# Performance work log

Measured on AMD Instinct MI355X. Metric: run time of the kernel, lower is better.

## Reference

```python
import jax, jax.numpy as jnp
import numpy as np

# CondInst DynamicMaskHead dims (defaults from cfg)
N_IMG, C_IN, H, W = 2, 8, 100, 152
N_INST = 500
CHANNELS = 8
STRIDE = 8  # mask_feat_stride (P3)
WEIGHT_NUMS = [(C_IN + 2) * CHANNELS, CHANNELS * CHANNELS, CHANNELS]  # [80, 64, 8]
BIAS_NUMS = [CHANNELS, CHANNELS, 1]
NUM_PARAMS = sum(WEIGHT_NUMS) + sum(BIAS_NUMS)  # 169


def setup_inputs() -> dict:
    key = jax.random.key(0)
    k1, k2, k3, k4, k5 = jax.random.split(key, 5)
    mask_feats = jax.random.normal(k1, (N_IMG, C_IN, H, W), jnp.float32)
    mask_head_params = jax.random.normal(k2, (N_INST, NUM_PARAMS), jnp.float32) * 0.1
    # instance centers in input-image pixel coords
    instance_locations = jax.random.uniform(k3, (N_INST, 2), jnp.float32) * jnp.array([W * STRIDE, H * STRIDE], jnp.float32)
    # sizes_of_interest gathered per instance fpn level (values in [64, 512])
    soi = jax.random.uniform(k4, (N_INST,), jnp.float32) * 448.0 + 64.0
    im_inds = jax.random.randint(k5, (N_INST,), 0, N_IMG)
    return {"mask_feats": mask_feats, "mask_head_params": mask_head_params,
            "instance_locations": instance_locations, "soi": soi, "im_inds": im_inds}


def compute_locations(h, w, stride):
    # matches adet compute_locations: center of each stride cell
    sx = jnp.arange(w, dtype=jnp.float32) * stride + stride // 2
    sy = jnp.arange(h, dtype=jnp.float32) * stride + stride // 2
    gy, gx = jnp.meshgrid(sy, sx, indexing="ij")
    return jnp.stack([gx.ravel(), gy.ravel()], axis=1)  # [H*W, 2] as (x, y)


def parse_dynamic_params(params):
    # faithful to parse_dynamic_params: split weights then biases along dim 1
    sizes = WEIGHT_NUMS + BIAS_NUMS
    splits = jnp.split(params, np.cumsum(sizes)[:-1].tolist(), axis=1)
    w0 = splits[0].reshape(N_INST, CHANNELS, C_IN + 2)   # layer0: (C_in+2)->channels
    w1 = splits[1].reshape(N_INST, CHANNELS, CHANNELS)   # layer1: channels->channels
    w2 = splits[2].reshape(N_INST, 1, CHANNELS)          # layer2: channels->1
    b0, b1, b2 = splits[3], splits[4], splits[5]
    return (w0, w1, w2), (b0, b1, b2)


def reference(mask_feats, mask_head_params, instance_locations, soi, im_inds):
    locations = compute_locations(H, W, STRIDE)  # [HW, 2]
    # relative coords: [n_inst, HW, 2] -> [n_inst, 2, HW], normalized by soi
    rel = (instance_locations[:, None, :] - locations[None, :, :]) / soi[:, None, None]
    rel = jnp.transpose(rel, (0, 2, 1)).astype(mask_feats.dtype)
    feats = mask_feats[im_inds].reshape(N_INST, C_IN, H * W)
    x = jnp.concatenate([rel, feats], axis=1)  # [n_inst, C_in+2, HW]
    (w0, w1, w2), (b0, b1, b2) = parse_dynamic_params(mask_head_params)
    # grouped 1x1 convs (groups=n_inst) == per-instance GEMM over pixels
    x = jax.nn.relu(jnp.einsum("noi,nip->nop", w0, x) + b0[:, :, None])
    x = jax.nn.relu(jnp.einsum("noi,nip->nop", w1, x) + b1[:, :, None])
    x = jnp.einsum("noi,nip->nop", w2, x) + b2[:, :, None]
    return x.reshape(N_INST, 1, H, W)  # mask_logits
```

## Files before the change

kernel.cpp:

```cpp
#include <hip/hip_runtime.h>

#define HGT 100
#define WID 152
#define HW (HGT * WID)
#define NINST 500
#define CIN 8
#define CH 8
#define NPARAMS 169
#define PPT 4


typedef float v4f __attribute__((ext_vector_type(4)));

static __device__ __forceinline__ v4f vsplat(float x) {
    v4f r = {x, x, x, x};
    return r;
}

static __device__ __forceinline__ v4f vfma(v4f a, v4f b, v4f c) {
#if __has_builtin(__builtin_elementwise_fma)
    return __builtin_elementwise_fma(a, b, c);
#else
    return a * b + c;
#endif
}

static __device__ __forceinline__ v4f vrelu(v4f a) {
#if __has_builtin(__builtin_elementwise_max)
    return __builtin_elementwise_max(a, vsplat(0.0f));
#else
    v4f r;
    r.x = fmaxf(a.x, 0.f); r.y = fmaxf(a.y, 0.f);
    r.z = fmaxf(a.z, 0.f); r.w = fmaxf(a.w, 0.f);
    return r;
#endif
}

__global__ __launch_bounds__(256, 4) void dyn_mask_head(
    const float* __restrict__ feats,
    const float* __restrict__ params,
    const float* __restrict__ locs,
    const float* __restrict__ soi,
    const int*  __restrict__ im_inds,
    float* __restrict__ out)
{
    const int n    = blockIdx.y;
    const int quad = blockIdx.x * blockDim.x + threadIdx.x;
    const int p0   = quad * PPT;
    if (p0 >= HW) return;

    const int   im      = im_inds[n];
    const float lx      = locs[n * 2 + 0];
    const float ly      = locs[n * 2 + 1];
    const float inv_soi = 1.0f / soi[n];
    const float* __restrict__ P = params + n * NPARAMS;

    const int py  = p0 / WID;
    const int px0 = p0 - py * WID;
    const float rely = (ly - (float)(py * 8 + 4)) * inv_soi;

    v4f relx;
#pragma unroll
    for (int r = 0; r < PPT; ++r)
        relx[r] = (lx - (float)((px0 + r) * 8 + 4)) * inv_soi;

    v4f f[CIN];
    const float* fb = feats + (size_t)im * CIN * HW + p0;
#pragma unroll
    for (int j = 0; j < CIN; ++j) {
        const float4 v = *reinterpret_cast<const float4*>(fb + (size_t)j * HW);
        v4f t = {v.x, v.y, v.z, v.w};
        f[j] = t;
    }

    v4f h0[CH];
#pragma unroll
    for (int c = 0; c < CH; ++c) {
        const float s = fmaf(P[c * 10 + 1], rely, P[152 + c]);
        v4f acc = vfma(vsplat(P[c * 10 + 0]), relx, vsplat(s));
#pragma unroll
        for (int i = 0; i < CIN; ++i)
            acc = vfma(vsplat(P[c * 10 + 2 + i]), f[i], acc);
        h0[c] = vrelu(acc);
    }

    v4f h1[CH];
#pragma unroll
    for (int c = 0; c < CH; ++c) {
        v4f acc = vfma(vsplat(P[80 + c * 8]), h0[0], vsplat(P[160 + c]));
#pragma unroll
        for (int i = 1; i < CH; ++i)
            acc = vfma(vsplat(P[80 + c * 8 + i]), h0[i], acc);
        h1[c] = vrelu(acc);
    }

    v4f o = vfma(vsplat(P[144]), h1[0], vsplat(P[168]));
#pragma unroll
    for (int i = 1; i < CH; ++i)
        o = vfma(vsplat(P[144 + i]), h1[i], o);

    float4 ov;
    ov.x = o[0]; ov.y = o[1]; ov.z = o[2]; ov.w = o[3];
    *reinterpret_cast<float4*>(out + (size_t)n * HW + p0) = ov;
}

extern "C" void kernel_launch(void* const* d_in, const int* in_sizes, int n_in,
                              void* d_out, int out_size, void* d_ws, size_t ws_size,
                              hipStream_t stream) {
    const float* feats   = (const float*)d_in[0];
    const float* params  = (const float*)d_in[1];
    const float* locs    = (const float*)d_in[2];
    const float* soi     = (const float*)d_in[3];
    const int*   im_inds = (const int*)d_in[4];
    float*       out     = (float*)d_out;

    const int quads_per_inst = HW / PPT;
    dim3 block(256);
    dim3 grid((quads_per_inst + block.x - 1) / block.x, NINST);
    dyn_mask_head<<<grid, block, 0, stream>>>(feats, params, locs, soi, im_inds, out);
}
```

Baseline: 32.07 us.

## Use packed fp16 dot2 instructions for the per-pixel MLP with LDS-staged weights

Moves the per-instance weights into shared memory as packed fp16 pairs, and converts the features and intermediate activations to packed fp16. Each pair of input channels then reduces with a single v_dot2_f32_f16 that accumulates in fp32. This roughly halves the VALU instruction count of the compute-bound 1x1 conv chain. In exchange it adds a block-wide barrier, an LDS staging step, and fp16 rounding of weights and activations (round toward zero), which lowers accuracy and could overflow for large activations.

Result: slower. 33.08 us (+3.2%).

```diff
diff --git a/kernel.cpp b/kernel.cpp
--- a/kernel.cpp
+++ b/kernel.cpp
@@ -1,4 +1,5 @@
 #include <hip/hip_runtime.h>
+#include <stdint.h>
 
 #define HGT 100
 #define WID 152
@@ -10,31 +11,38 @@
 #define PPT 4
 
 
-typedef float v4f __attribute__((ext_vector_type(4)));
+typedef __fp16 h2 __attribute__((ext_vector_type(2)));
 
-static __device__ __forceinline__ v4f vsplat(float x) {
-    v4f r = {x, x, x, x};
+static __device__ __forceinline__ float dot2(h2 a, h2 b, float c) {
+#if __has_builtin(__builtin_amdgcn_fdot2)
+    return __builtin_amdgcn_fdot2(a, b, c, false);
+#else
+    float r = c;
+    asm("v_dot2_f32_f16 %0, %1, %2, %0" : "+v"(r) : "v"(a), "v"(b));
     return r;
-}
-
-static __device__ __forceinline__ v4f vfma(v4f a, v4f b, v4f c) {
-#if __has_builtin(__builtin_elementwise_fma)
-    return __builtin_elementwise_fma(a, b, c);
-#else
-    return a * b + c;
 #endif
 }
 
-static __device__ __forceinline__ v4f vrelu(v4f a) {
+static __device__ __forceinline__ h2 pkrtz(float lo, float hi) {
+    return __builtin_amdgcn_cvt_pkrtz(lo, hi);
+}
+
+static __device__ __forceinline__ h2 hrelu(h2 a) {
+    h2 z = {(__fp16)0.0f, (__fp16)0.0f};
 #if __has_builtin(__builtin_elementwise_max)
-    return __builtin_elementwise_max(a, vsplat(0.0f));
+    return __builtin_elementwise_max(a, z);
 #else
-    v4f r;
-    r.x = fmaxf(a.x, 0.f); r.y = fmaxf(a.y, 0.f);
-    r.z = fmaxf(a.z, 0.f); r.w = fmaxf(a.w, 0.f);
+    h2 r;
+    r.x = a.x > (__fp16)0.0f ? a.x : (__fp16)0.0f;
+    r.y = a.y > (__fp16)0.0f ? a.y : (__fp16)0.0f;
     return r;
 #endif
 }
+
+static __device__ __forceinline__ h2 bc(uint32_t u) {
+    return __builtin_bit_cast(h2, u);
+}
+
 
 __global__ __launch_bounds__(256, 4) void dyn_mask_head(
     const float* __restrict__ feats,
@@ -44,64 +52,121 @@
     const int*  __restrict__ im_inds,
     float* __restrict__ out)
 {
-    const int n    = blockIdx.y;
-    const int quad = blockIdx.x * blockDim.x + threadIdx.x;
-    const int p0   = quad * PPT;
-    if (p0 >= HW) return;
+    __shared__ __align__(16) uint32_t wpk[68];
 
-    const int   im      = im_inds[n];
-    const float lx      = locs[n * 2 + 0];
-    const float ly      = locs[n * 2 + 1];
-    const float inv_soi = 1.0f / soi[n];
+    const int n = blockIdx.y;
+    const int t = threadIdx.x;
     const float* __restrict__ P = params + n * NPARAMS;
 
-    const int py  = p0 / WID;
-    const int px0 = p0 - py * WID;
-    const float rely = (ly - (float)(py * 8 + 4)) * inv_soi;
+    if (t < 68) {
+        int src;
+        if (t < 32)      src = (t >> 2) * 10 + 2 + 2 * (t & 3);
+        else if (t < 64) src = 80 + 2 * (t - 32);
+        else             src = 144 + 2 * (t - 64);
+        wpk[t] = __builtin_bit_cast(uint32_t, pkrtz(P[src], P[src + 1]));
+    }
+    __syncthreads();
 
-    v4f relx;
+    const int q  = blockIdx.x * blockDim.x + t;
+    const int p0 = q * PPT;
+    if (p0 < HW) {
+        const int   im      = im_inds[n];
+        const float lx      = locs[n * 2 + 0];
+        const float ly      = locs[n * 2 + 1];
+        const float inv_soi = 1.0f / soi[n];
+
+        const int py  = p0 / WID;
+        const int px0 = p0 - py * WID;
+        const float rely = (ly - (float)(py * 8 + 4)) * inv_soi;
+        float relx[PPT];
 #pragma unroll
-    for (int r = 0; r < PPT; ++r)
-        relx[r] = (lx - (float)((px0 + r) * 8 + 4)) * inv_soi;
+        for (int r = 0; r < PPT; ++r)
+            relx[r] = (lx - (float)((px0 + r) * 8 + 4)) * inv_soi;
 
-    v4f f[CIN];
-    const float* fb = feats + (size_t)im * CIN * HW + p0;
+        h2 fpk[4][PPT];
+        const float* fb = feats + (size_t)im * CIN * HW + p0;
 #pragma unroll
-    for (int j = 0; j < CIN; ++j) {
-        const float4 v = *reinterpret_cast<const float4*>(fb + (size_t)j * HW);
-        v4f t = {v.x, v.y, v.z, v.w};
-        f[j] = t;
+        for (int m = 0; m < 4; ++m) {
+            const float4 va = *reinterpret_cast<const float4*>(fb + (size_t)(2 * m) * HW);
+            const float4 vb = *reinterpret_cast<const float4*>(fb + (size_t)(2 * m + 1) * HW);
+            fpk[m][0] = pkrtz(va.x, vb.x);
+            fpk[m][1] = pkrtz(va.y, vb.y);
+            fpk[m][2] = pkrtz(va.z, vb.z);
+            fpk[m][3] = pkrtz(va.w, vb.w);
+        }
+
+        h2 h0pk[4][PPT];
+#pragma unroll
+        for (int m = 0; m < 4; ++m) {
+            const int c0 = 2 * m, c1 = 2 * m + 1;
+            const uint4 wa = *reinterpret_cast<const uint4*>(&wpk[4 * c0]);
+            const uint4 wb = *reinterpret_cast<const uint4*>(&wpk[4 * c1]);
+            const float sa = fmaf(P[c0 * 10 + 1], rely, P[152 + c0]);
+            const float sb = fmaf(P[c1 * 10 + 1], rely, P[152 + c1]);
+            float aa[PPT], ab[PPT];
+#pragma unroll
+            for (int r = 0; r < PPT; ++r) {
+                float x = fmaf(P[c0 * 10 + 0], relx[r], sa);
+                x = dot2(bc(wa.x), fpk[0][r], x);
+                x = dot2(bc(wa.y), fpk[1][r], x);
+                x = dot2(bc(wa.z), fpk[2][r], x);
+                x = dot2(bc(wa.w), fpk[3][r], x);
+                aa[r] = x;
+                float y = fmaf(P[c1 * 10 + 0], relx[r], sb);
+                y = dot2(bc(wb.x), fpk[0][r], y);
+                y = dot2(bc(wb.y), fpk[1][r], y);
+                y = dot2(bc(wb.z), fpk[2][r], y);
+                y = dot2(bc(wb.w), fpk[3][r], y);
+                ab[r] = y;
+            }
+#pragma unroll
+            for (int r = 0; r < PPT; ++r)
+                h0pk[m][r] = hrelu(pkrtz(aa[r], ab[r]));
+        }
+
+        h2 h1pk[4][PPT];
+#pragma unroll
+        for (int m = 0; m < 4; ++m) {
+            const int c0 = 2 * m, c1 = 2 * m + 1;
+            const uint4 wa = *reinterpret_cast<const uint4*>(&wpk[32 + 4 * c0]);
+            const uint4 wb = *reinterpret_cast<const uint4*>(&wpk[32 + 4 * c1]);
+            const float ba = P[160 + c0];
+            const float bb = P[160 + c1];
+            float aa[PPT], ab[PPT];
+#pragma unroll
+            for (int r = 0; r < PPT; ++r) {
+                float x = dot2(bc(wa.x), h0pk[0][r], ba);
+                x = dot2(bc(wa.y), h0pk[1][r], x);
+                x = dot2(bc(wa.z), h0pk[2][r], x);
+                x = dot2(bc(wa.w), h0pk[3][r], x);
+                aa[r] = x;
+                float y = dot2(bc(wb.x), h0pk[0][r], bb);
+                y = dot2(bc(wb.y), h0pk[1][r], y);
+                y = dot2(bc(wb.z), h0pk[2][r], y);
+                y = dot2(bc(wb.w), h0pk[3][r], y);
+                ab[r] = y;
+            }
+#pragma unroll
+            for (int r = 0; r < PPT; ++r)
+                h1pk[m][r] = hrelu(pkrtz(aa[r], ab[r]));
+        }
+
+        const uint4 w2 = *reinterpret_cast<const uint4*>(&wpk[64]);
+        const float b2 = P[168];
+        float o[PPT];
+#pragma unroll
+        for (int r = 0; r < PPT; ++r) {
+            float x = dot2(bc(w2.x), h1pk[0][r], b2);
+            x = dot2(bc(w2.y), h1pk[1][r], x);
+            x = dot2(bc(w2.z), h1pk[2][r], x);
+            x = dot2(bc(w2.w), h1pk[3][r], x);
+            o[r] = x;
+        }
+
+        float4 ov;
+        ov.x = o[0]; ov.y = o[1]; ov.z = o[2]; ov.w = o[3];
+        *reinterpret_cast<float4*>(out + (size_t)n * HW + p0) = ov;
     }
-
-    v4f h0[CH];
-#pragma unroll
-    for (int c = 0; c < CH; ++c) {
-        const float s = fmaf(P[c * 10 + 1], rely, P[152 + c]);
-        v4f acc = vfma(vsplat(P[c * 10 + 0]), relx, vsplat(s));
-#pragma unroll
-        for (int i = 0; i < CIN; ++i)
-            acc = vfma(vsplat(P[c * 10 + 2 + i]), f[i], acc);
-        h0[c] = vrelu(acc);
-    }
-
-    v4f h1[CH];
-#pragma unroll
-    for (int c = 0; c < CH; ++c) {
-        v4f acc = vfma(vsplat(P[80 + c * 8]), h0[0], vsplat(P[160 + c]));
-#pragma unroll
-        for (int i = 1; i < CH; ++i)
-            acc = vfma(vsplat(P[80 + c * 8 + i]), h0[i], acc);
-        h1[c] = vrelu(acc);
-    }
-
-    v4f o = vfma(vsplat(P[144]), h1[0], vsplat(P[168]));
-#pragma unroll
-    for (int i = 1; i < CH; ++i)
-        o = vfma(vsplat(P[144 + i]), h1[i], o);
-
-    float4 ov;
-    ov.x = o[0]; ov.y = o[1]; ov.z = o[2]; ov.w = o[3];
-    *reinterpret_cast<float4*>(out + (size_t)n * HW + p0) = ov;
 }
 
 extern "C" void kernel_launch(void* const* d_in, const int* in_sizes, int n_in,
```
